# Performance work log

Hardware: AMD Instinct MI355X
Metric: run time of the kernel (lower is better)

Reference implementation:

```python
import jax, jax.numpy as jnp
import numpy as np

B, A, U, S, E, H = 32768, 8, 64, 512, 128, 4
HYP = 256  # unused (two_hyper_layers=False)
COEF = 0.001
NEG = -99999999.0


def setup_inputs() -> dict:
    key = jax.random.key(0)
    ks = jax.random.split(key, 11)
    def lin(k, shape, fan_in):
        return jax.random.normal(k, shape, dtype=jnp.float32) * (1.0 / np.sqrt(fan_in))
    return {
        "agent_qs": jax.random.normal(ks[0], (B, A), dtype=jnp.float32),
        "states": jax.random.normal(ks[1], (B, S), dtype=jnp.float32),
        "actions": jax.random.randint(ks[2], (B, A), 0, 10, dtype=jnp.int64),
        "W_sel": lin(ks[3], (H, E, S), S),        # per-head selector extractor (no bias)
        "W_key": lin(ks[4], (H, E, U + 1), U + 1),  # per-head key extractor (no bias)
        "Wv1": lin(ks[5], (E, S), S),
        "bv1": jnp.zeros((E,), dtype=jnp.float32),
        "Wv2": lin(ks[6], (1, E), E),
        "bv2": jnp.zeros((1,), dtype=jnp.float32),
        "Wh": lin(ks[7], (H, S), S),              # hyper_w_head
        "bh": jnp.zeros((H,), dtype=jnp.float32),
    }


def reference(agent_qs, states, actions, W_sel, W_key, Wv1, bv1, Wv2, bv2, Wh, bh):
    b = states.shape[0]
    unit = states[:, : U * A].reshape(b, A, U)                     # [B,A,U]
    x = jnp.concatenate([unit, agent_qs[:, :, None]], axis=2)       # [B,A,U+1] (nonlinear)
    sel = jnp.einsum('bs,hes->bhe', states, W_sel)                  # all-head selectors
    keys = jnp.einsum('bau,heu->bhae', x, W_key)                    # all-head keys
    logits = jnp.einsum('bhe,bhae->bha', sel, keys)                 # attend_logits per head
    scaled = logits / np.float32(np.sqrt(E))
    dead = (actions == 0)[:, None, :]                               # mask_dead
    scaled = jnp.where(dead, NEG, scaled)
    weights = jax.nn.softmax(scaled, axis=2)                        # [B,H,A]
    v = jax.nn.relu(states @ Wv1.T + bv1) @ Wv2.T + bv2             # [B,1]
    w_head = jnp.abs(states @ Wh.T + bh)                            # [B,H] weighted_head
    head_attend = jnp.sum(weights * w_head[:, :, None], axis=1)     # [B,A]
    attend_mag_regs = COEF * jnp.sum(jnp.mean(logits ** 2, axis=(0, 2)))
    head_entropies = -jnp.mean(jnp.sum(jnp.log(weights + 1e-8) * weights, axis=2), axis=0)  # [H]
    return head_attend, v, attend_mag_regs, head_entropies
```

## Files before the change

kernel.cpp:

```cpp
#include <hip/hip_runtime.h>


typedef unsigned short u16;
typedef unsigned int u32;
typedef float f32x4 __attribute__((ext_vector_type(4)));
typedef short s16x8 __attribute__((ext_vector_type(8)));
typedef unsigned int u32x4 __attribute__((ext_vector_type(4)));
typedef unsigned int u32x2 __attribute__((ext_vector_type(2)));

#define NEGV -99999999.0f
#define CSTRIDE 424

__device__ __forceinline__ u16 f2bf(float f) {
  union { float f; u32 u; } v; v.f = f;
  u32 r = v.u + 0x7fffu + ((v.u >> 16) & 1u);
  return (u16)(r >> 16);
}
__device__ __forceinline__ float bfl(u32 w) { union { u32 u; float f; } v; v.u = w << 16; return v.f; }
__device__ __forceinline__ float bfh(u32 w) { union { u32 u; float f; } v; v.u = w & 0xffff0000u; return v.f; }

__device__ __forceinline__ void panel_store(u16* Wp, int p, int s, float v) {
  Wp[(s >> 5) * 12800 + p * 32 + (s & 31)] = f2bf(v);
}

__global__ __launch_bounds__(256) void kprep(
    const float* __restrict__ Wsel, const float* __restrict__ Wkey,
    const float* __restrict__ Wv1, const float* __restrict__ Wh,
    u16* __restrict__ Wp, float* __restrict__ accs) {
  const int bid = blockIdx.x, t = threadIdx.x;
  if (bid < 128) {
    __shared__ float wsS[2048];
    __shared__ float wkS[8320];
    const int h = bid >> 5, s0 = (bid & 31) << 4;
    for (int i = t; i < 2048; i += 256)
      wsS[i] = Wsel[((size_t)h * 128 + (i >> 4)) * 512 + s0 + (i & 15)];
    for (int i = t; i < 8320; i += 256)
      wkS[i] = Wkey[(size_t)h * 8320 + i];
    __syncthreads();
    {
      const int u = t >> 2, sl0 = (t & 3) << 2;
      float a0 = 0.f, a1 = 0.f, a2 = 0.f, a3 = 0.f;
      for (int e = 0; e < 128; ++e) {
        const float k = wkS[e * 65 + u];
        const float* wr = wsS + e * 16 + sl0;
        a0 = fmaf(k, wr[0], a0); a1 = fmaf(k, wr[1], a1);
        a2 = fmaf(k, wr[2], a2); a3 = fmaf(k, wr[3], a3);
      }
      const int p = h * 64 + u, s = s0 + sl0;
      panel_store(Wp, p, s, a0);     panel_store(Wp, p, s + 1, a1);
      panel_store(Wp, p, s + 2, a2); panel_store(Wp, p, s + 3, a3);
    }
    if (t < 16) {
      float a = 0.f;
      for (int e = 0; e < 128; ++e)
        a = fmaf(wkS[e * 65 + 64], wsS[e * 16 + t], a);
      panel_store(Wp, 256 + h, s0 + t, a);
    }
  } else {
    if (bid == 128 && t < 16) accs[t] = 0.f;
    for (int row = 260 + (bid - 128); row < 400; row += 8) {
      for (int s = t; s < 512; s += 256) {
        float v = 0.f;
        if (row >= 264 && row < 392) v = Wv1[(row - 264) * 512 + s];
        else if (row >= 392 && row < 396) v = Wh[(row - 392) * 512 + s];
        panel_store(Wp, row, s, v);
      }
    }
  }
}

__device__ __forceinline__ void stageA(unsigned char* dst, const float4& x0, const float4& x1) {
  u32x4 aw;
  aw[0] = (u32)f2bf(x0.x) | ((u32)f2bf(x0.y) << 16);
  aw[1] = (u32)f2bf(x0.z) | ((u32)f2bf(x0.w) << 16);
  aw[2] = (u32)f2bf(x1.x) | ((u32)f2bf(x1.y) << 16);
  aw[3] = (u32)f2bf(x1.z) | ((u32)f2bf(x1.w) << 16);
  *(u32x4*)dst = aw;
}

__global__ __launch_bounds__(256, 2) void kmain(
    const float* __restrict__ states, const float* __restrict__ agent_qs,
    const int* __restrict__ actions, const u16* __restrict__ Wp,
    const float* __restrict__ bv1, const float* __restrict__ Wv2,
    const float* __restrict__ bv2, const float* __restrict__ bh,
    float* __restrict__ out, float* __restrict__ accs) {
  __shared__ __align__(16) unsigned char smem[65536 + 80];
  u16* const Ctile = (u16*)smem;
  float* const red = (float*)(smem + 65536);

  const int tid = threadIdx.x;
  const int wid = tid >> 6;
  const int lane = tid & 63;
  const int c16 = lane & 15, sq = lane >> 4;
  const int slot = sq ^ ((c16 >> 1) & 3);
  const int b0 = blockIdx.x * 64;

  const f32x4 zf = {0.f, 0.f, 0.f, 0.f};
  f32x4 acc[4][7];
#pragma unroll
  for (int r = 0; r < 4; ++r)
#pragma unroll
    for (int i = 0; i < 7; ++i) acc[r][i] = zf;

  const int ar = tid >> 2, ac = tid & 3;
  const float* aG = states + (size_t)(b0 + ar) * 512 + ac * 8;
  const int aWoff = ar * 64 + ((ac ^ ((ar >> 1) & 3)) << 4);
#pragma unroll
  for (int kt = 0; kt < 16; ++kt) {
    float4 x0 = *(const float4*)(aG + kt * 32);
    float4 x1 = *(const float4*)(aG + kt * 32 + 4);
    stageA(smem + kt * 4096 + aWoff, x0, x1);
  }
  __syncthreads();

  const u16* bQ[7];
#pragma unroll
  for (int i = 0; i < 7; ++i) {
    const int f = wid + (i << 2);
    bQ[i] = Wp + ((f < 25 ? f : 0) * 16 + c16) * 32 + sq * 8;
  }

#pragma unroll
  for (int kt = 0; kt < 16; ++kt) {
    s16x8 bfr[7];
#pragma unroll
    for (int i = 0; i < 7; ++i)
      if (wid + (i << 2) < 25)
        bfr[i] = *(const s16x8*)(bQ[i] + kt * 12800);
    s16x8 af[4];
#pragma unroll
    for (int r = 0; r < 4; ++r)
      af[r] = *(const s16x8*)(smem + kt * 4096 + (r * 16 + c16) * 64 + slot * 16);
#pragma unroll
    for (int i = 0; i < 7; ++i)
      if (wid + (i << 2) < 25) {
#pragma unroll
        for (int r = 0; r < 4; ++r)
          acc[r][i] = __builtin_amdgcn_mfma_f32_16x16x32_bf16(
              af[r], bfr[i], acc[r][i], 0, 0, 0);
      }
  }
  __syncthreads();

#pragma unroll
  for (int r = 0; r < 4; ++r)
#pragma unroll
    for (int i = 0; i < 7; ++i) {
      const int f = wid + (i << 2);
      if (f < 25) {
        const int col = (f << 4) + c16;
        const int rowb = (r << 4) + (sq << 2);
#pragma unroll
        for (int j = 0; j < 4; ++j)
          Ctile[(rowb + j) * CSTRIDE + col] = f2bf(acc[r][i][j]);
      }
    }
  __syncthreads();

  const int rloc = (wid << 4) + c16;
  const int b = b0 + rloc;
  const int qt = sq;
  const u16* crow = Ctile + rloc * CSTRIDE;
  const float* srow = states + (size_t)b * 512;

  float m[4][16];
#pragma unroll
  for (int h = 0; h < 4; ++h) {
    u32x4 w0 = *(const u32x4*)(crow + h * 64 + qt * 16);
    u32x4 w1 = *(const u32x4*)(crow + h * 64 + qt * 16 + 8);
#pragma unroll
    for (int k = 0; k < 4; ++k) {
      m[h][2 * k] = bfl(w0[k]);     m[h][2 * k + 1] = bfh(w0[k]);
      m[h][8 + 2 * k] = bfl(w1[k]); m[h][8 + 2 * k + 1] = bfh(w1[k]);
    }
  }

  float lp[4][8];
#pragma unroll
  for (int h = 0; h < 4; ++h)
#pragma unroll
    for (int a = 0; a < 8; ++a) lp[h][a] = 0.f;

#pragma unroll
  for (int a = 0; a < 8; ++a) {
    const float* xp = srow + a * 64 + qt * 16;
    float4 v0 = *(const float4*)(xp);
    float4 v1 = *(const float4*)(xp + 4);
    float4 v2 = *(const float4*)(xp + 8);
    float4 v3 = *(const float4*)(xp + 12);
    float xv[16] = {v0.x, v0.y, v0.z, v0.w, v1.x, v1.y, v1.z, v1.w,
                    v2.x, v2.y, v2.z, v2.w, v3.x, v3.y, v3.z, v3.w};
#pragma unroll
    for (int h = 0; h < 4; ++h) {
      float s = 0.f;
#pragma unroll
      for (int t2 = 0; t2 < 16; ++t2) s = fmaf(m[h][t2], xv[t2], s);
      lp[h][a] += s;
    }
  }
#pragma unroll
  for (int h = 0; h < 4; ++h)
#pragma unroll
    for (int a = 0; a < 8; ++a) {
      float v = lp[h][a];
      v += __shfl_xor(v, 16, 64);
      v += __shfl_xor(v, 32, 64);
      lp[h][a] = v;
    }
  float4 q0 = *(const float4*)(agent_qs + (size_t)b * 8);
  float4 q1 = *(const float4*)(agent_qs + (size_t)b * 8 + 4);
  float qv[8] = {q0.x, q0.y, q0.z, q0.w, q1.x, q1.y, q1.z, q1.w};
  u32x2 w64 = *(const u32x2*)(crow + 256);
  float m64[4] = {bfl(w64[0]), bfh(w64[0]), bfl(w64[1]), bfh(w64[1])};
#pragma unroll
  for (int h = 0; h < 4; ++h)
#pragma unroll
    for (int a = 0; a < 8; ++a) lp[h][a] = fmaf(m64[h], qv[a], lp[h][a]);

  float magp = 0.f;
  if (qt == 0) {
#pragma unroll
    for (int h = 0; h < 4; ++h)
#pragma unroll
      for (int a = 0; a < 8; ++a) magp = fmaf(lp[h][a], lp[h][a], magp);
  }
  float bvv[32], wvv[32], cv[32];
#pragma unroll
  for (int g = 0; g < 8; ++g) {
    *(float4*)(bvv + g * 4) = *(const float4*)(bv1 + qt * 32 + g * 4);
    *(float4*)(wvv + g * 4) = *(const float4*)(Wv2 + qt * 32 + g * 4);
  }
#pragma unroll
  for (int g = 0; g < 4; ++g) {
    u32x4 wv = *(const u32x4*)(crow + 264 + qt * 32 + g * 8);
#pragma unroll
    for (int k = 0; k < 4; ++k) {
      cv[g * 8 + 2 * k] = bfl(wv[k]); cv[g * 8 + 2 * k + 1] = bfh(wv[k]);
    }
  }
  float vp = 0.f;
#pragma unroll
  for (int e2 = 0; e2 < 32; ++e2)
    vp = fmaf(fmaxf(cv[e2] + bvv[e2], 0.f), wvv[e2], vp);
  vp += __shfl_xor(vp, 16, 64);
  vp += __shfl_xor(vp, 32, 64);

  int av[8];
  const int* ap = actions + (size_t)b * 8;
#pragma unroll
  for (int a = 0; a < 8; ++a) av[a] = ap[a];

  u32x2 ww = *(const u32x2*)(crow + 392);
  float whr[4] = {bfl(ww[0]), bfh(ww[0]), bfl(ww[1]), bfh(ww[1])};
  float4 bh4 = *(const float4*)(bh);
  float bhv[4] = {bh4.x, bh4.y, bh4.z, bh4.w};

  const float scale = 0.088388347648318447f;
  float att[8];
#pragma unroll
  for (int a = 0; a < 8; ++a) att[a] = 0.f;
  float entp[4];
#pragma unroll
  for (int h = 0; h < 4; ++h) {
    float whv = fabsf(whr[h] + bhv[h]);
    float sc[8];
#pragma unroll
    for (int a = 0; a < 8; ++a)
      sc[a] = (av[a] == 0) ? NEGV : lp[h][a] * scale;
    float mx = sc[0];
#pragma unroll
    for (int a = 1; a < 8; ++a) mx = fmaxf(mx, sc[a]);
    float ex[8];
    float sum = 0.f;
#pragma unroll
    for (int a = 0; a < 8; ++a) { ex[a] = __expf(sc[a] - mx); sum += ex[a]; }
    float inv = 1.f / sum;
    float ent = 0.f;
#pragma unroll
    for (int a = 0; a < 8; ++a) {
      float w = ex[a] * inv;
      att[a] = fmaf(w, whv, att[a]);
      ent = fmaf(w, __logf(w + 1e-8f), ent);
    }
    entp[h] = ent;
  }

  if (qt == 0) {
    float4 o0 = {att[0], att[1], att[2], att[3]};
    float4 o1 = {att[4], att[5], att[6], att[7]};
    *(float4*)(out + (size_t)b * 8) = o0;
    *(float4*)(out + (size_t)b * 8 + 4) = o1;
    out[262144 + b] = vp + bv2[0];
  }

  float r0 = magp;
  float r1 = (qt == 0) ? entp[0] : 0.f;
  float r2 = (qt == 0) ? entp[1] : 0.f;
  float r3 = (qt == 0) ? entp[2] : 0.f;
  float r4 = (qt == 0) ? entp[3] : 0.f;
#pragma unroll
  for (int off = 1; off < 64; off <<= 1) {
    r0 += __shfl_xor(r0, off, 64);
    r1 += __shfl_xor(r1, off, 64);
    r2 += __shfl_xor(r2, off, 64);
    r3 += __shfl_xor(r3, off, 64);
    r4 += __shfl_xor(r4, off, 64);
  }
  if (lane == 0) {
    red[wid * 5 + 0] = r0; red[wid * 5 + 1] = r1; red[wid * 5 + 2] = r2;
    red[wid * 5 + 3] = r3; red[wid * 5 + 4] = r4;
  }
  __syncthreads();
  if (tid < 5) {
    float s = red[tid] + red[5 + tid] + red[10 + tid] + red[15 + tid];
    atomicAdd(&accs[tid], s);
  }
  __syncthreads();
  if (tid == 0) {
    u32* cnt = (u32*)(accs + 8);
    if (atomicAdd(cnt, 1u) == 511u) {
      float a0 = atomicAdd(&accs[0], 0.f);
      float a1 = atomicAdd(&accs[1], 0.f);
      float a2 = atomicAdd(&accs[2], 0.f);
      float a3 = atomicAdd(&accs[3], 0.f);
      float a4 = atomicAdd(&accs[4], 0.f);
      out[294912] = 0.001f * a0 * (1.0f / 262144.0f);
      out[294913] = -a1 * (1.0f / 32768.0f);
      out[294914] = -a2 * (1.0f / 32768.0f);
      out[294915] = -a3 * (1.0f / 32768.0f);
      out[294916] = -a4 * (1.0f / 32768.0f);
    }
  }
}

extern "C" void kernel_launch(void* const* d_in, const int* in_sizes, int n_in,
                              void* d_out, int out_size, void* d_ws, size_t ws_size,
                              hipStream_t stream) {
  const float* agent_qs = (const float*)d_in[0];
  const float* states   = (const float*)d_in[1];
  const int*   actions  = (const int*)d_in[2];
  const float* Wsel = (const float*)d_in[3];
  const float* Wkey = (const float*)d_in[4];
  const float* Wv1  = (const float*)d_in[5];
  const float* bv1  = (const float*)d_in[6];
  const float* Wv2  = (const float*)d_in[7];
  const float* bv2  = (const float*)d_in[8];
  const float* Wh   = (const float*)d_in[9];
  const float* bh   = (const float*)d_in[10];
  float* out = (float*)d_out;
  float* accs = (float*)d_ws;
  u16* Wp = (u16*)((char*)d_ws + 64);

  hipLaunchKernelGGL(kprep, dim3(136), dim3(256), 0, stream,
                     Wsel, Wkey, Wv1, Wh, Wp, accs);
  hipLaunchKernelGGL(kmain, dim3(512), dim3(256), 0, stream,
                     states, agent_qs, actions, Wp, bv1, Wv2, bv2, bh, out, accs);
}
```

Before: 64.59 us.

## Double-buffer GEMM K-loop with async global-to-LDS loads for A and B

The main GEMM loop now streams both the fp32 states tile and the bf16 weight panel into double-buffered LDS using global_load_lds, overlapping the next K-tile's loads with the current tile's MFMAs. The weight panel layout is padded and pre-swizzled in the prep kernel so that direct LDS copies land in a bank-conflict-friendly layout. fp32-to-bf16 conversion of the activations moves from a staging pass into the compute step. In exchange there are two barriers per iteration and extra conversion ALU work inside the loop, and LDS use grows, which may affect how many blocks fit per CU.

```diff
diff --git a/kernel.cpp b/kernel.cpp
--- a/kernel.cpp
+++ b/kernel.cpp
@@ -7,9 +7,12 @@
 typedef short s16x8 __attribute__((ext_vector_type(8)));
 typedef unsigned int u32x4 __attribute__((ext_vector_type(4)));
 typedef unsigned int u32x2 __attribute__((ext_vector_type(2)));
+typedef __attribute__((address_space(1))) const u32 gu32;
+typedef __attribute__((address_space(3))) u32 lu32;
 
 #define NEGV -99999999.0f
 #define CSTRIDE 424
+#define PKTB 28672
 
 __device__ __forceinline__ u16 f2bf(float f) {
   union { float f; u32 u; } v; v.f = f;
@@ -20,7 +23,8 @@
 __device__ __forceinline__ float bfh(u32 w) { union { u32 u; float f; } v; v.u = w & 0xffff0000u; return v.f; }
 
 __device__ __forceinline__ void panel_store(u16* Wp, int p, int s, float v) {
-  Wp[(s >> 5) * 12800 + p * 32 + (s & 31)] = f2bf(v);
+  const int kt = s >> 5, c = (s >> 3) & 3, j = s & 7;
+  Wp[kt * 14336 + p * 32 + ((c ^ ((p >> 1) & 3)) << 3) + j] = f2bf(v);
 }
 
 __global__ __launch_bounds__(256) void kprep(
@@ -58,7 +62,7 @@
     }
   } else {
     if (bid == 128 && t < 16) accs[t] = 0.f;
-    for (int row = 260 + (bid - 128); row < 400; row += 8) {
+    for (int row = 260 + (bid - 128); row < 448; row += 8) {
       for (int s = t; s < 512; s += 256) {
         float v = 0.f;
         if (row >= 264 && row < 392) v = Wv1[(row - 264) * 512 + s];
@@ -69,13 +73,47 @@
   }
 }
 
-__device__ __forceinline__ void stageA(unsigned char* dst, const float4& x0, const float4& x1) {
-  u32x4 aw;
-  aw[0] = (u32)f2bf(x0.x) | ((u32)f2bf(x0.y) << 16);
-  aw[1] = (u32)f2bf(x0.z) | ((u32)f2bf(x0.w) << 16);
-  aw[2] = (u32)f2bf(x1.x) | ((u32)f2bf(x1.y) << 16);
-  aw[3] = (u32)f2bf(x1.z) | ((u32)f2bf(x1.w) << 16);
-  *(u32x4*)dst = aw;
+__device__ __forceinline__ void stage_tile(
+    unsigned char* bufB, unsigned char* bufA, const char* wpB,
+    const float* pA0, const float* pA1, int wid) {
+#pragma unroll
+  for (int i = 0; i < 7; ++i) {
+    const int c = wid + (i << 2);
+    __builtin_amdgcn_global_load_lds((gu32*)(wpB + c * 1024),
+                                     (lu32*)(bufB + c * 1024), 16, 0, 0);
+  }
+  __builtin_amdgcn_global_load_lds((gu32*)pA0, (lu32*)(bufA + wid * 1024), 16, 0, 0);
+  __builtin_amdgcn_global_load_lds((gu32*)pA1, (lu32*)(bufA + (wid + 4) * 1024), 16, 0, 0);
+}
+
+__device__ __forceinline__ void computeT(const unsigned char* bufA,
+                                         const unsigned char* bufB,
+                                         int wid, int c16, int sq,
+                                         f32x4 acc[4][7]) {
+  const int slotB = sq ^ ((c16 >> 1) & 3);
+  const int swz = c16 & 7;
+  s16x8 af[4];
+#pragma unroll
+  for (int r = 0; r < 4; ++r) {
+    const unsigned char* rb = bufA + (r * 16 + c16) * 128;
+    f32x4 wa = *(const f32x4*)(rb + (((2 * sq) ^ swz) << 4));
+    f32x4 wb = *(const f32x4*)(rb + (((2 * sq + 1) ^ swz) << 4));
+    af[r][0] = (short)f2bf(wa[0]); af[r][1] = (short)f2bf(wa[1]);
+    af[r][2] = (short)f2bf(wa[2]); af[r][3] = (short)f2bf(wa[3]);
+    af[r][4] = (short)f2bf(wb[0]); af[r][5] = (short)f2bf(wb[1]);
+    af[r][6] = (short)f2bf(wb[2]); af[r][7] = (short)f2bf(wb[3]);
+  }
+#pragma unroll
+  for (int i = 0; i < 7; ++i) {
+    const int f = wid + (i << 2);
+    if (f < 25) {
+      s16x8 bfr = *(const s16x8*)(bufB + (f * 16 + c16) * 64 + slotB * 16);
+#pragma unroll
+      for (int r = 0; r < 4; ++r)
+        acc[r][i] = __builtin_amdgcn_mfma_f32_16x16x32_bf16(
+            af[r], bfr, acc[r][i], 0, 0, 0);
+    }
+  }
 }
 
 __global__ __launch_bounds__(256, 2) void kmain(
@@ -84,15 +122,18 @@
     const float* __restrict__ bv1, const float* __restrict__ Wv2,
     const float* __restrict__ bv2, const float* __restrict__ bh,
     float* __restrict__ out, float* __restrict__ accs) {
-  __shared__ __align__(16) unsigned char smem[65536 + 80];
+  __shared__ __align__(16) unsigned char smem[73728 + 80];
+  unsigned char* const B0 = smem;
+  unsigned char* const B1 = smem + 28672;
+  unsigned char* const A0 = smem + 57344;
+  unsigned char* const A1 = smem + 65536;
   u16* const Ctile = (u16*)smem;
-  float* const red = (float*)(smem + 65536);
+  float* const red = (float*)(smem + 73728);
 
   const int tid = threadIdx.x;
   const int wid = tid >> 6;
   const int lane = tid & 63;
   const int c16 = lane & 15, sq = lane >> 4;
-  const int slot = sq ^ ((c16 >> 1) & 3);
   const int b0 = blockIdx.x * 64;
 
   const f32x4 zf = {0.f, 0.f, 0.f, 0.f};
@@ -102,44 +143,33 @@
 #pragma unroll
     for (int i = 0; i < 7; ++i) acc[r][i] = zf;
 
-  const int ar = tid >> 2, ac = tid & 3;
-  const float* aG = states + (size_t)(b0 + ar) * 512 + ac * 8;
-  const int aWoff = ar * 64 + ((ac ^ ((ar >> 1) & 3)) << 4);
-#pragma unroll
-  for (int kt = 0; kt < 16; ++kt) {
-    float4 x0 = *(const float4*)(aG + kt * 32);
-    float4 x1 = *(const float4*)(aG + kt * 32 + 4);
-    stageA(smem + kt * 4096 + aWoff, x0, x1);
-  }
-  __syncthreads();
-
-  const u16* bQ[7];
-#pragma unroll
-  for (int i = 0; i < 7; ++i) {
-    const int f = wid + (i << 2);
-    bQ[i] = Wp + ((f < 25 ? f : 0) * 16 + c16) * 32 + sq * 8;
-  }
-
-#pragma unroll
-  for (int kt = 0; kt < 16; ++kt) {
-    s16x8 bfr[7];
-#pragma unroll
-    for (int i = 0; i < 7; ++i)
-      if (wid + (i << 2) < 25)
-        bfr[i] = *(const s16x8*)(bQ[i] + kt * 12800);
-    s16x8 af[4];
-#pragma unroll
-    for (int r = 0; r < 4; ++r)
-      af[r] = *(const s16x8*)(smem + kt * 4096 + (r * 16 + c16) * 64 + slot * 16);
-#pragma unroll
-    for (int i = 0; i < 7; ++i)
-      if (wid + (i << 2) < 25) {
-#pragma unroll
-        for (int r = 0; r < 4; ++r)
-          acc[r][i] = __builtin_amdgcn_mfma_f32_16x16x32_bf16(
-              af[r], bfr[i], acc[r][i], 0, 0, 0);
-      }
-  }
+  const int rowoff = lane >> 3;
+  const int xslot = (lane & 7) ^ rowoff;
+  const float* pA0 = states + (size_t)(b0 + 8 * wid + rowoff) * 512 + xslot * 4;
+  const float* pA1 = pA0 + 32 * 512;
+  const char* const wpB = (const char*)Wp + lane * 16;
+
+  stage_tile(B0, A0, wpB, pA0, pA1, wid);
+  asm volatile("s_waitcnt vmcnt(0)" ::: "memory");
+  __builtin_amdgcn_s_barrier();
+
+  for (int kt = 0; kt < 15; ++kt) {
+    unsigned char* const sbB = (kt & 1) ? B0 : B1;
+    unsigned char* const sbA = (kt & 1) ? A0 : A1;
+    const unsigned char* const cbB = (kt & 1) ? B1 : B0;
+    const unsigned char* const cbA = (kt & 1) ? A1 : A0;
+    stage_tile(sbB, sbA, wpB + (size_t)(kt + 1) * PKTB,
+               pA0 + (kt + 1) * 32, pA1 + (kt + 1) * 32, wid);
+    __builtin_amdgcn_sched_barrier(0);
+    asm volatile("s_waitcnt vmcnt(9)" ::: "memory");
+    __builtin_amdgcn_s_barrier();
+    computeT(cbA, cbB, wid, c16, sq, acc);
+    __builtin_amdgcn_sched_barrier(0);
+    __builtin_amdgcn_s_barrier();
+  }
+  asm volatile("s_waitcnt vmcnt(0)" ::: "memory");
+  __builtin_amdgcn_s_barrier();
+  computeT(A1, B1, wid, c16, sq, acc);
   __syncthreads();
 
 #pragma unroll
```

New measurement: 64.09 us. Within noise of the previous version (-0.8%).
